# Kernel optimization log

Measured on AMD Instinct MI355X. Metric: run time of the kernel, lower is better.

## Reference

```python
import jax, jax.numpy as jnp
import numpy as np
import math

B, S, D_IN, D_ATTN, D_HID = 4, 2048, 1024, 1024, 1024

def gelu_erf(x):
    return 0.5 * x * (1.0 + jax.lax.erf(x / math.sqrt(2.0)))

def setup_inputs() -> dict:
    key = jax.random.key(0)
    k = jax.random.split(key, 8)
    inputs = jax.random.normal(k[0], (B, S, D_IN), dtype=jnp.float32)
    attn_mask = jax.random.randint(k[1], (B, S, S), 0, 2, dtype=jnp.int32)
    sq = 1.0 / math.sqrt(D_IN)
    Wq = jax.random.normal(k[2], (D_IN, D_ATTN), dtype=jnp.float32) * sq
    bq = jnp.zeros((D_ATTN,), dtype=jnp.float32)
    Wk = jax.random.normal(k[3], (D_IN, D_ATTN), dtype=jnp.float32) * sq
    bk = jnp.zeros((D_ATTN,), dtype=jnp.float32)
    Wv = jax.random.normal(k[4], (D_IN, D_HID), dtype=jnp.float32) * sq
    bv = jnp.zeros((D_HID,), dtype=jnp.float32)
    return {"inputs": inputs, "attn_mask": attn_mask,
            "Wq": Wq, "bq": bq, "Wk": Wk, "bk": bk, "Wv": Wv, "bv": bv}

def reference(inputs, attn_mask, Wq, bq, Wk, bk, Wv, bv):
    # Q, K: [B, S, d_k]
    Q = inputs @ Wq + bq
    K = inputs @ Wk + bk
    scores = jnp.einsum('bqd,bkd->bqk', Q, K) / math.sqrt(D_ATTN)
    scores = scores + attn_mask.astype(scores.dtype) * (-1e9)
    attn = jax.nn.softmax(scores, axis=-1)
    WV = gelu_erf(inputs @ Wv + bv)           # [B, S, hidden]
    context = jnp.einsum('bqk,bkh->bqh', attn, WV)
    return (context, attn)
```

## Files before the change

### kernel.cpp

```cpp
#include <hip/hip_runtime.h>
#include <hip/hip_bf16.h>
#include <math.h>

#define B_   4
#define S_   2048
#define DIN  1024
#define DATT 1024
#define DHID 1024

typedef short bf16x8 __attribute__((ext_vector_type(8)));
typedef float f32x4  __attribute__((ext_vector_type(4)));

__device__ inline unsigned short f2bf(float f) {
    unsigned u = __float_as_uint(f);
    u += 0x7fffu + ((u >> 16) & 1u);
    return (unsigned short)(u >> 16);
}
__device__ inline float bf2f(unsigned u16) {
    return __uint_as_float(u16 << 16);
}
__device__ inline void gld16(const void* g, void* l) {
    __builtin_amdgcn_global_load_lds(
        (const __attribute__((address_space(1))) unsigned int*)g,
        (__attribute__((address_space(3))) unsigned int*)l, 16, 0, 0);
}

__global__ __launch_bounds__(256)
void xcvt_k(const float* __restrict__ x, unsigned short* __restrict__ xb)
{
    int i = blockIdx.x * 256 + threadIdx.x;
    const float4* p = (const float4*)x + (size_t)i * 2;
    float4 v0 = p[0], v1 = p[1];
    uint4 o;
    o.x = (unsigned)f2bf(v0.x) | ((unsigned)f2bf(v0.y) << 16);
    o.y = (unsigned)f2bf(v0.z) | ((unsigned)f2bf(v0.w) << 16);
    o.z = (unsigned)f2bf(v1.x) | ((unsigned)f2bf(v1.y) << 16);
    o.w = (unsigned)f2bf(v1.z) | ((unsigned)f2bf(v1.w) << 16);
    ((uint4*)xb)[i] = o;
}

__global__ __launch_bounds__(256)
void wcvt_k(const float* __restrict__ Wq, const float* __restrict__ Wk,
            const float* __restrict__ Wv, unsigned short* __restrict__ Wt)
{
    int w = blockIdx.y;
    const float* W = (w == 0) ? Wq : ((w == 1) ? Wk : Wv);
    unsigned short* D = Wt + (size_t)w * DIN * DATT;
    int t = blockIdx.x * 256 + threadIdx.x;
    int n  = t >> 6;
    int kc = (t & 63) * 16;
    unsigned short r[16];
#pragma unroll
    for (int i = 0; i < 16; ++i) r[i] = f2bf(W[(size_t)(kc + i) * DATT + n]);
    uint4 o0, o1;
    o0.x = (unsigned)r[0] | ((unsigned)r[1] << 16);  o0.y = (unsigned)r[2] | ((unsigned)r[3] << 16);
    o0.z = (unsigned)r[4] | ((unsigned)r[5] << 16);  o0.w = (unsigned)r[6] | ((unsigned)r[7] << 16);
    o1.x = (unsigned)r[8] | ((unsigned)r[9] << 16);  o1.y = (unsigned)r[10] | ((unsigned)r[11] << 16);
    o1.z = (unsigned)r[12] | ((unsigned)r[13] << 16); o1.w = (unsigned)r[14] | ((unsigned)r[15] << 16);
    *(uint4*)(D + (size_t)n * DIN + kc)     = o0;
    *(uint4*)(D + (size_t)n * DIN + kc + 8) = o1;
}

template<int EPI>
__global__ __launch_bounds__(512, 2)
void gemm256_k(const unsigned short* __restrict__ Ap, const unsigned short* __restrict__ Bp,
               const float* __restrict__ b0, const float* __restrict__ b1,
               const float* __restrict__ b2, const int* __restrict__ maskp,
               void* __restrict__ Cp, void* __restrict__ Cp2,
               int K, int lda, int ldb, int ldc,
               long aStride, long bStride, long cStride, long mStride, float scale)
{
    __shared__ __align__(16) char ldsb[131072];

    const int tid  = threadIdx.x;
    const int z    = blockIdx.z;
    const int row0 = blockIdx.y * 256;
    const int col0 = blockIdx.x * 256;
    const int wid  = tid >> 6, lane = tid & 63;
    const int lr = lane & 15, lg = lane >> 4;
    const int wm = wid >> 2, wn = wid & 3;
    const int tw = (tid & 448) * 16;

    const unsigned short* Ab = Ap + (size_t)aStride * z;
    const unsigned short* Bb = Bp + (size_t)bStride * z;

    const int swzA = lr & 7;
    const int swzB = lg ^ ((lr >> 1) & 3);

    f32x4 acc[8][4] = {};
    const int nt = K >> 6;

#define STAGE_A(buf, k0n, r) {                                                  \
    int gr = (((r) & 1) << 7) + (((r) >> 1) << 6) + (tid >> 3);                 \
    int jj = (tid & 7) ^ (gr & 7);                                              \
    gld16(Ab + (size_t)(row0 + gr) * lda + (k0n) + jj * 8,                      \
          ldsb + (size_t)(buf) * 65536 + (r) * 8192 + tw); }

#define STAGE_B(buf, k0n, r) {                                                  \
    int rw = (((r) & 1) << 7) + (tid >> 2);                                     \
    int jj = (tid & 3) ^ ((rw >> 1) & 3);                                       \
    gld16(Bb + (size_t)(col0 + rw) * ldb + (k0n) + ((r) >> 1) * 32 + jj * 8,    \
          ldsb + (size_t)(buf) * 65536 + 32768 + ((r) >> 1) * 16384             \
               + (((r) & 1) << 13) + tw); }

#define PHASE(mh, kk, DOSTAGE) {                                                \
    const char* lb = ldsb + (size_t)cb * 65536;                                 \
    bf16x8 av[4], bv[4];                                                        \
    _Pragma("unroll")                                                           \
    for (int m = 0; m < 4; ++m) {                                               \
        int Rl = (mh) * 128 + wm * 64 + m * 16 + lr;                            \
        av[m] = *(const bf16x8*)(lb + Rl * 128 + ((((kk) * 4 + lg) ^ swzA) * 16)); \
    }                                                                           \
    _Pragma("unroll")                                                           \
    for (int n = 0; n < 4; ++n) {                                               \
        int Rb = wn * 64 + n * 16 + lr;                                         \
        bv[n] = *(const bf16x8*)(lb + 32768 + (kk) * 16384 + Rb * 64 + swzB * 16); \
    }                                                                           \
    DOSTAGE;                                                                    \
    asm volatile("s_waitcnt lgkmcnt(0)" ::: "memory");                          \
    __builtin_amdgcn_sched_barrier(0);                                          \
    __builtin_amdgcn_s_setprio(1);                                              \
    _Pragma("unroll")                                                           \
    for (int m = 0; m < 4; ++m)                                                 \
        _Pragma("unroll")                                                       \
        for (int n = 0; n < 4; ++n)                                             \
            acc[(mh) * 4 + m][n] = __builtin_amdgcn_mfma_f32_16x16x32_bf16(     \
                av[m], bv[n], acc[(mh) * 4 + m][n], 0, 0, 0);                   \
    __builtin_amdgcn_s_setprio(0); }

    STAGE_A(0, 0, 0); STAGE_B(0, 0, 0);
    STAGE_A(0, 0, 1); STAGE_B(0, 0, 1);
    STAGE_A(0, 0, 2); STAGE_A(0, 0, 3);
    STAGE_B(0, 0, 2); STAGE_B(0, 0, 3);

    int cb = 0;
    for (int t = 0; t < nt; ++t) {
        const bool pf = (t + 1) < nt;
        const int k0n = (t + 1) << 6;
        const int nb = cb ^ 1;
        asm volatile("s_waitcnt vmcnt(4)\ns_barrier" ::: "memory");
        PHASE(0, 0, if (pf) { STAGE_A(nb, k0n, 0); STAGE_B(nb, k0n, 0); })
        if (pf) asm volatile("s_waitcnt vmcnt(4)\ns_barrier" ::: "memory");
        else    asm volatile("s_waitcnt vmcnt(2)\ns_barrier" ::: "memory");
        PHASE(1, 0, if (pf) { STAGE_A(nb, k0n, 1); STAGE_B(nb, k0n, 1); })
        if (pf) asm volatile("s_waitcnt vmcnt(4)\ns_barrier" ::: "memory");
        else    asm volatile("s_waitcnt vmcnt(0)\ns_barrier" ::: "memory");
        PHASE(0, 1, if (pf) { STAGE_A(nb, k0n, 2); STAGE_A(nb, k0n, 3); })
        PHASE(1, 1, if (pf) { STAGE_B(nb, k0n, 2); STAGE_B(nb, k0n, 3); })
        cb = nb;
    }
#undef PHASE
#undef STAGE_A
#undef STAGE_B

    if (EPI == 6) {
        int w = col0 >> 10;
        int cb0 = (col0 & 1023) + wn * 64;
        if (w < 2) {
            unsigned short* C = (unsigned short*)Cp + (size_t)w * ((size_t)B_ * S_ * DATT);
            const float* bias = w ? b1 : b0;
#pragma unroll
            for (int ni = 0; ni < 4; ++ni) {
                int col = cb0 + ni * 16 + lr;
                float bb = bias[col];
#pragma unroll
                for (int mi = 0; mi < 8; ++mi) {
                    int rowb = row0 + wm * 128 + mi * 16 + lg * 4;
#pragma unroll
                    for (int v = 0; v < 4; ++v)
                        C[(size_t)(rowb + v) * DATT + col] = f2bf(acc[mi][ni][v] + bb);
                }
            }
        } else {
            unsigned short* C = (unsigned short*)Cp2;
            int zz = row0 >> 11;
            int sb = (row0 & 2047) + wm * 128;
#pragma unroll
            for (int ni = 0; ni < 4; ++ni) {
                int col = cb0 + ni * 16 + lr;
                float bb = b2[col];
#pragma unroll
                for (int mi = 0; mi < 8; ++mi) {
                    unsigned short r[4];
#pragma unroll
                    for (int v = 0; v < 4; ++v) {
                        float xv = acc[mi][ni][v] + bb;
                        xv = 0.5f * xv * (1.0f + erff(xv * 0.70710678118654752f));
                        r[v] = f2bf(xv);
                    }
                    uint2 o;
                    o.x = (unsigned)r[0] | ((unsigned)r[1] << 16);
                    o.y = (unsigned)r[2] | ((unsigned)r[3] << 16);
                    *(uint2*)(C + ((size_t)zz * DHID + col) * S_ + sb + mi * 16 + lg * 4) = o;
                }
            }
        }
    } else if (EPI == 4) {
        unsigned short* C = (unsigned short*)Cp + (size_t)cStride * z;
        const int* mp = maskp + (size_t)mStride * z;
#pragma unroll
        for (int mi = 0; mi < 8; ++mi) {
            int rowb = row0 + wm * 128 + mi * 16 + lg * 4;
#pragma unroll
            for (int ni = 0; ni < 4; ++ni) {
                int col = col0 + wn * 64 + ni * 16 + lr;
#pragma unroll
                for (int v = 0; v < 4; ++v) {
                    float sv = acc[mi][ni][v] * scale;
                    int mk = mp[(size_t)(rowb + v) * ldc + col];
                    float ev = mk ? 0.0f : __expf(sv);
                    C[(size_t)(rowb + v) * ldc + col] = f2bf(ev);
                }
            }
        }
    } else {
        float* C = (float*)Cp + (size_t)cStride * z;
        const float* invs = b0 + (size_t)z * S_;
#pragma unroll
        for (int mi = 0; mi < 8; ++mi) {
            int rowb = row0 + wm * 128 + mi * 16 + lg * 4;
#pragma unroll
            for (int ni = 0; ni < 4; ++ni) {
                int col = col0 + wn * 64 + ni * 16 + lr;
#pragma unroll
                for (int v = 0; v < 4; ++v)
                    C[(size_t)(rowb + v) * ldc + col] = acc[mi][ni][v] * invs[rowb + v];
            }
        }
    }
}

template<bool WRITEATTN>
__global__ __launch_bounds__(256)
void rownorm_k(const unsigned short* __restrict__ e, float* __restrict__ attn,
               float* __restrict__ invs)
{
    const int row = blockIdx.x;
    const int tid = threadIdx.x;
    uint4 u = ((const uint4*)(e + (size_t)row * S_))[tid];
    float f[8];
    f[0] = bf2f(u.x & 0xffffu); f[1] = bf2f(u.x >> 16);
    f[2] = bf2f(u.y & 0xffffu); f[3] = bf2f(u.y >> 16);
    f[4] = bf2f(u.z & 0xffffu); f[5] = bf2f(u.z >> 16);
    f[6] = bf2f(u.w & 0xffffu); f[7] = bf2f(u.w >> 16);
    float s = ((f[0] + f[1]) + (f[2] + f[3])) + ((f[4] + f[5]) + (f[6] + f[7]));
#pragma unroll
    for (int o = 32; o; o >>= 1) s += __shfl_xor(s, o);
    __shared__ float red[4];
    if ((tid & 63) == 0) red[tid >> 6] = s;
    __syncthreads();
    s = (red[0] + red[1]) + (red[2] + red[3]);
    float inv = 1.0f / s;
    if (WRITEATTN) {
        float* p = attn + (size_t)row * S_;
        ((float4*)p)[tid * 2]     = make_float4(f[0] * inv, f[1] * inv, f[2] * inv, f[3] * inv);
        ((float4*)p)[tid * 2 + 1] = make_float4(f[4] * inv, f[5] * inv, f[6] * inv, f[7] * inv);
    } else {
        if (tid == 0) invs[row] = inv;
    }
}

template<int AMODE, int EPI>
__global__ __launch_bounds__(256)
void gemm_k(const void* __restrict__ Ap, const unsigned short* __restrict__ Bp,
            const float* __restrict__ b0, const float* __restrict__ b1,
            const float* __restrict__ b2, const int* __restrict__ maskp,
            void* __restrict__ Cp, void* __restrict__ Cp2,
            int K, int lda, int ldb, int ldc,
            long aStride, long bStride, long cStride, long mStride, float scale)
{
    __shared__ __align__(16) unsigned short sh[2][2][128][64];
    const int tid  = threadIdx.x;
    const int z    = blockIdx.z;
    const int row0 = blockIdx.y * 128;
    const int col0 = blockIdx.x * 128;
    const int wave = tid >> 6, lane = tid & 63;
    const int lr = lane & 15, lg = lane >> 4;
    const int wm = (wave >> 1) * 64, wn = (wave & 1) * 64;
    const unsigned short* Bb = Bp + (size_t)bStride * z;
    f32x4 acc[4][4] = {};
    const int nt = K >> 6;
    auto stage = [&](int b, int k0) {
        if (AMODE == 0) {
            const unsigned short* A = (const unsigned short*)Ap + (size_t)aStride * z;
#pragma unroll
            for (int q = 0; q < 4; ++q) {
                int c = q * 256 + tid;
                int row = c >> 3, j = c & 7;
                gld16((const char*)(A + (size_t)(row0 + row) * lda + k0) + ((j ^ (row & 7)) << 4),
                      (char*)&sh[b][0][0][0] + ((q * 256 + (tid & 192)) << 4));
            }
        } else {
            const float* A = (const float*)Ap + (size_t)aStride * z;
#pragma unroll
            for (int q = 0; q < 4; ++q) {
                int c = q * 256 + tid;
                int row = c >> 3, j = c & 7;
                const float* src = A + (size_t)(row0 + row) * lda + k0 + ((j ^ (row & 7)) << 3);
                float4 v0 = *(const float4*)src;
                float4 v1 = *(const float4*)(src + 4);
                uint4 p;
                p.x = (unsigned)f2bf(v0.x) | ((unsigned)f2bf(v0.y) << 16);
                p.y = (unsigned)f2bf(v0.z) | ((unsigned)f2bf(v0.w) << 16);
                p.z = (unsigned)f2bf(v1.x) | ((unsigned)f2bf(v1.y) << 16);
                p.w = (unsigned)f2bf(v1.z) | ((unsigned)f2bf(v1.w) << 16);
                *(uint4*)((char*)&sh[b][0][0][0] + ((size_t)c << 4)) = p;
            }
        }
#pragma unroll
        for (int q = 0; q < 4; ++q) {
            int c = q * 256 + tid;
            int row = c >> 3, j = c & 7;
            gld16((const char*)(Bb + (size_t)(col0 + row) * ldb + k0) + ((j ^ (row & 7)) << 4),
                  (char*)&sh[b][1][0][0] + ((q * 256 + (tid & 192)) << 4));
        }
    };
    stage(0, 0);
    __syncthreads();
    int cur = 0;
    for (int t = 0; t < nt; ++t) {
        if (t + 1 < nt) stage(cur ^ 1, (t + 1) << 6);
        const char* baseA = (const char*)&sh[cur][0][0][0];
        const char* baseB = (const char*)&sh[cur][1][0][0];
        bf16x8 af[2][4], bfv[2][4];
#pragma unroll
        for (int s = 0; s < 2; ++s)
#pragma unroll
            for (int i = 0; i < 4; ++i) {
                int ra = wm + i * 16 + lr;
                af[s][i]  = *(const bf16x8*)(baseA + ra * 128 + ((((s << 2) | lg) ^ (ra & 7)) << 4));
                int rb = wn + i * 16 + lr;
                bfv[s][i] = *(const bf16x8*)(baseB + rb * 128 + ((((s << 2) | lg) ^ (rb & 7)) << 4));
            }
#pragma unroll
        for (int s = 0; s < 2; ++s)
#pragma unroll
            for (int mi = 0; mi < 4; ++mi)
#pragma unroll
                for (int ni = 0; ni < 4; ++ni)
                    acc[mi][ni] = __builtin_amdgcn_mfma_f32_16x16x32_bf16(af[s][mi], bfv[s][ni], acc[mi][ni], 0, 0, 0);
        if (t + 1 < nt) __syncthreads();
        cur ^= 1;
    }
    if (EPI == 6) {
        int w = col0 >> 10;
        int cb = (col0 & 1023) + wn;
        if (w < 2) {
            unsigned short* C = (unsigned short*)Cp + (size_t)w * ((size_t)B_ * S_ * DATT);
            const float* bias = w ? b1 : b0;
#pragma unroll
            for (int mi = 0; mi < 4; ++mi)
#pragma unroll
                for (int ni = 0; ni < 4; ++ni) {
                    int col = cb + ni * 16 + lr;
                    float bb = bias[col];
                    int rowb = row0 + wm + mi * 16 + lg * 4;
#pragma unroll
                    for (int v = 0; v < 4; ++v)
                        C[(size_t)(rowb + v) * DATT + col] = f2bf(acc[mi][ni][v] + bb);
                }
        } else {
            unsigned short* C = (unsigned short*)Cp2;
            int zz = row0 >> 11;
            int sb = (row0 & 2047) + wm;
#pragma unroll
            for (int mi = 0; mi < 4; ++mi)
#pragma unroll
                for (int ni = 0; ni < 4; ++ni) {
                    int col = cb + ni * 16 + lr;
                    float bb = b2[col];
                    unsigned short r[4];
#pragma unroll
                    for (int v = 0; v < 4; ++v) {
                        float xv = acc[mi][ni][v] + bb;
                        xv = 0.5f * xv * (1.0f + erff(xv * 0.70710678118654752f));
                        r[v] = f2bf(xv);
                    }
                    uint2 o;
                    o.x = (unsigned)r[0] | ((unsigned)r[1] << 16);
                    o.y = (unsigned)r[2] | ((unsigned)r[3] << 16);
                    *(uint2*)(C + ((size_t)zz * DHID + col) * S_ + sb + mi * 16 + lg * 4) = o;
                }
        }
    } else {
        float* C = (float*)Cp + (size_t)cStride * z;
        const int* mp = (EPI == 2) ? (maskp + (size_t)mStride * z) : nullptr;
#pragma unroll
        for (int mi = 0; mi < 4; ++mi)
#pragma unroll
            for (int ni = 0; ni < 4; ++ni) {
                int col = col0 + wn + ni * 16 + lr;
                int rowb = row0 + wm + mi * 16 + lg * 4;
#pragma unroll
                for (int v = 0; v < 4; ++v) {
                    float val = acc[mi][ni][v];
                    if (EPI == 2) val = val * scale + (float)mp[(size_t)(rowb + v) * ldc + col] * (-1e9f);
                    C[(size_t)(rowb + v) * ldc + col] = val;
                }
            }
    }
}

__global__ __launch_bounds__(256)
void softmax_k(float* __restrict__ attn)
{
    const int row = blockIdx.x;
    float* p = attn + (size_t)row * S_;
    const int tid = threadIdx.x;
    float4 a = ((const float4*)p)[tid * 2];
    float4 b = ((const float4*)p)[tid * 2 + 1];
    float m = fmaxf(fmaxf(fmaxf(a.x, a.y), fmaxf(a.z, a.w)),
                    fmaxf(fmaxf(b.x, b.y), fmaxf(b.z, b.w)));
#pragma unroll
    for (int o = 32; o; o >>= 1) m = fmaxf(m, __shfl_xor(m, o));
    __shared__ float redm[4];
    __shared__ float reds[4];
    if ((tid & 63) == 0) redm[tid >> 6] = m;
    __syncthreads();
    m = fmaxf(fmaxf(redm[0], redm[1]), fmaxf(redm[2], redm[3]));
    float e[8];
    e[0] = expf(a.x - m); e[1] = expf(a.y - m); e[2] = expf(a.z - m); e[3] = expf(a.w - m);
    e[4] = expf(b.x - m); e[5] = expf(b.y - m); e[6] = expf(b.z - m); e[7] = expf(b.w - m);
    float s = e[0] + e[1] + e[2] + e[3] + e[4] + e[5] + e[6] + e[7];
#pragma unroll
    for (int o = 32; o; o >>= 1) s += __shfl_xor(s, o);
    if ((tid & 63) == 0) reds[tid >> 6] = s;
    __syncthreads();
    s = reds[0] + reds[1] + reds[2] + reds[3];
    float inv = 1.0f / s;
    ((float4*)p)[tid * 2]     = make_float4(e[0] * inv, e[1] * inv, e[2] * inv, e[3] * inv);
    ((float4*)p)[tid * 2 + 1] = make_float4(e[4] * inv, e[5] * inv, e[6] * inv, e[7] * inv);
}

extern "C" void kernel_launch(void* const* d_in, const int* in_sizes, int n_in,
                              void* d_out, int out_size, void* d_ws, size_t ws_size,
                              hipStream_t stream)
{
    const float* x    = (const float*)d_in[0];
    const int*   mask = (const int*)d_in[1];
    const float* Wq   = (const float*)d_in[2];
    const float* bq   = (const float*)d_in[3];
    const float* Wk   = (const float*)d_in[4];
    const float* bk   = (const float*)d_in[5];
    const float* Wv   = (const float*)d_in[6];
    const float* bv   = (const float*)d_in[7];

    float* ctx  = (float*)d_out;
    float* attn = ctx + (size_t)B_ * S_ * DHID;

    unsigned short* Qb = (unsigned short*)ctx;
    unsigned short* Kb = Qb + (size_t)B_ * S_ * DATT;
    unsigned short* Xb   = (unsigned short*)attn;
    unsigned short* Wb   = Xb + (size_t)B_ * S_ * DIN;
    unsigned short* WVbT = Wb + (size_t)3 * DIN * DATT;

    const size_t eElems = (size_t)B_ * S_ * S_;
    bool fast = ws_size >= eElems * 2 + (size_t)B_ * S_ * 4 + 256;

    dim3 blk(256), blk5(512);

    xcvt_k<<<dim3(4096), blk, 0, stream>>>(x, Xb);
    wcvt_k<<<dim3(256, 3), blk, 0, stream>>>(Wq, Wk, Wv, Wb);

    if (fast) {
        unsigned short* e    = (unsigned short*)d_ws;
        float*          invs = (float*)(e + eElems);

        gemm256_k<6><<<dim3(12, 32, 1), blk5, 0, stream>>>(
            Xb, Wb, bq, bk, bv, nullptr, Qb, WVbT,
            DIN, DIN, DIN, 0, 0, 0, 0, 0, 1.0f);
        gemm256_k<4><<<dim3(8, 8, 4), blk5, 0, stream>>>(
            Qb, Kb, nullptr, nullptr, nullptr, mask, e, nullptr,
            DATT, DATT, DATT, S_,
            (long)S_ * DATT, (long)S_ * DATT, (long)S_ * S_, (long)S_ * S_, 0.03125f);
        rownorm_k<false><<<dim3(B_ * S_), blk, 0, stream>>>(e, nullptr, invs);
        gemm256_k<5><<<dim3(4, 8, 4), blk5, 0, stream>>>(
            e, WVbT, invs, nullptr, nullptr, nullptr, ctx, nullptr,
            S_, S_, S_, DHID,
            (long)S_ * S_, (long)DHID * S_, (long)S_ * DHID, 0, 1.0f);
        rownorm_k<true><<<dim3(B_ * S_), blk, 0, stream>>>(e, attn, nullptr);
    } else {
        unsigned short* WVw = (unsigned short*)d_ws;
        gemm_k<0, 6><<<dim3(24, 64, 1), blk, 0, stream>>>(
            Xb, Wb, bq, bk, bv, nullptr, Qb, WVw,
            DIN, DIN, DIN, 0, 0, 0, 0, 0, 1.0f);
        gemm_k<0, 2><<<dim3(16, 16, 4), blk, 0, stream>>>(
            Qb, Kb, nullptr, nullptr, nullptr, mask, attn, nullptr,
            DATT, DATT, DATT, S_,
            (long)S_ * DATT, (long)S_ * DATT, (long)S_ * S_, (long)S_ * S_, 0.03125f);
        softmax_k<<<dim3(B_ * S_), blk, 0, stream>>>(attn);
        gemm_k<1, 3><<<dim3(8, 16, 4), blk, 0, stream>>>(
            attn, WVw, nullptr, nullptr, nullptr, nullptr, ctx, nullptr,
            S_, S_, S_, DHID,
            (long)S_ * S_, (long)DHID * S_, (long)S_ * DHID, 0, 1.0f);
    }
}
```

Baseline: 243.0 us.

## Bit-pack attention mask, add 256x128 GEMM tile, reuse B fragments across phases

Adds a pre-pass that packs the int32 attention mask into one bit per element. The QK^T epilogue then reads 32x less mask data than the per-element int loads it replaces. The projection and context GEMMs move to a new 256x128 tile kernel with smaller LDS use, which doubles the grid size to fill more CUs. Both GEMM variants also reuse the B fragments loaded in the first M-half phase for the second, cutting redundant LDS reads. The costs are an extra kernel launch, more workspace, and lower per-block reuse in the narrower tile.

```diff
diff --git a/kernel.cpp b/kernel.cpp
--- a/kernel.cpp
+++ b/kernel.cpp
@@ -61,14 +61,28 @@
     *(uint4*)(D + (size_t)n * DIN + kc + 8) = o1;
 }
 
-template<int EPI>
+__global__ __launch_bounds__(256)
+void mpack_k(const int* __restrict__ m, unsigned* __restrict__ mb)
+{
+    int w = blockIdx.x * 256 + threadIdx.x;
+    const uint4* p = (const uint4*)(m + (size_t)w * 32);
+    unsigned bits = 0;
+#pragma unroll
+    for (int g = 0; g < 8; ++g) {
+        uint4 v = p[g];
+        bits |= (v.x ? 1u : 0u) << (g * 4 + 0);
+        bits |= (v.y ? 1u : 0u) << (g * 4 + 1);
+        bits |= (v.z ? 1u : 0u) << (g * 4 + 2);
+        bits |= (v.w ? 1u : 0u) << (g * 4 + 3);
+    }
+    mb[w] = bits;
+}
+
 __global__ __launch_bounds__(512, 2)
-void gemm256_k(const unsigned short* __restrict__ Ap, const unsigned short* __restrict__ Bp,
-               const float* __restrict__ b0, const float* __restrict__ b1,
-               const float* __restrict__ b2, const int* __restrict__ maskp,
-               void* __restrict__ Cp, void* __restrict__ Cp2,
-               int K, int lda, int ldb, int ldc,
-               long aStride, long bStride, long cStride, long mStride, float scale)
+void gemmA_k(const unsigned short* __restrict__ Ap, const unsigned short* __restrict__ Bp,
+             const unsigned* __restrict__ mbits, unsigned short* __restrict__ Cp,
+             int K, int lda, int ldb, int ldc,
+             long aStride, long bStride, long cStride, float scale)
 {
     __shared__ __align__(16) char ldsb[131072];
 
@@ -103,18 +117,20 @@
           ldsb + (size_t)(buf) * 65536 + 32768 + ((r) >> 1) * 16384             \
                + (((r) & 1) << 13) + tw); }
 
-#define PHASE(mh, kk, DOSTAGE) {                                                \
+#define PHASE_A(mh, kk, BV, LOADB, DOSTAGE) {                                   \
     const char* lb = ldsb + (size_t)cb * 65536;                                 \
-    bf16x8 av[4], bv[4];                                                        \
+    bf16x8 av[4];                                                               \
     _Pragma("unroll")                                                           \
     for (int m = 0; m < 4; ++m) {                                               \
         int Rl = (mh) * 128 + wm * 64 + m * 16 + lr;                            \
-        av[m] = *(const bf16x8*)(lb + Rl * 128 + ((((kk) * 4 + lg) ^ swzA) * 16)); \
+        av[m] = *(const bf16x8*)(lb + Rl * 128 + ((((kk) * 4 + lg) ^ swzA) << 4)); \
     }                                                                           \
-    _Pragma("unroll")                                                           \
-    for (int n = 0; n < 4; ++n) {                                               \
-        int Rb = wn * 64 + n * 16 + lr;                                         \
-        bv[n] = *(const bf16x8*)(lb + 32768 + (kk) * 16384 + Rb * 64 + swzB * 16); \
+    if (LOADB) {                                                                \
+        _Pragma("unroll")                                                       \
+        for (int n = 0; n < 4; ++n) {                                           \
+            int Rb = wn * 64 + n * 16 + lr;                                     \
+            BV[n] = *(const bf16x8*)(lb + 32768 + (kk) * 16384 + Rb * 64 + (swzB << 4)); \
+        }                                                                       \
     }                                                                           \
     DOSTAGE;                                                                    \
     asm volatile("s_waitcnt lgkmcnt(0)" ::: "memory");                          \
@@ -125,7 +141,7 @@
         _Pragma("unroll")                                                       \
         for (int n = 0; n < 4; ++n)                                             \
             acc[(mh) * 4 + m][n] = __builtin_amdgcn_mfma_f32_16x16x32_bf16(     \
-                av[m], bv[n], acc[(mh) * 4 + m][n], 0, 0, 0);                   \
+                av[m], BV[n], acc[(mh) * 4 + m][n], 0, 0, 0);                   \
     __builtin_amdgcn_s_setprio(0); }
 
     STAGE_A(0, 0, 0); STAGE_B(0, 0, 0);
@@ -138,20 +154,137 @@
         const bool pf = (t + 1) < nt;
         const int k0n = (t + 1) << 6;
         const int nb = cb ^ 1;
+        bf16x8 bv0[4], bv1[4];
         asm volatile("s_waitcnt vmcnt(4)\ns_barrier" ::: "memory");
-        PHASE(0, 0, if (pf) { STAGE_A(nb, k0n, 0); STAGE_B(nb, k0n, 0); })
+        PHASE_A(0, 0, bv0, true,  if (pf) { STAGE_A(nb, k0n, 0); STAGE_B(nb, k0n, 0); })
         if (pf) asm volatile("s_waitcnt vmcnt(4)\ns_barrier" ::: "memory");
         else    asm volatile("s_waitcnt vmcnt(2)\ns_barrier" ::: "memory");
-        PHASE(1, 0, if (pf) { STAGE_A(nb, k0n, 1); STAGE_B(nb, k0n, 1); })
+        PHASE_A(1, 0, bv0, false, if (pf) { STAGE_A(nb, k0n, 1); STAGE_B(nb, k0n, 1); })
         if (pf) asm volatile("s_waitcnt vmcnt(4)\ns_barrier" ::: "memory");
         else    asm volatile("s_waitcnt vmcnt(0)\ns_barrier" ::: "memory");
-        PHASE(0, 1, if (pf) { STAGE_A(nb, k0n, 2); STAGE_A(nb, k0n, 3); })
-        PHASE(1, 1, if (pf) { STAGE_B(nb, k0n, 2); STAGE_B(nb, k0n, 3); })
+        PHASE_A(0, 1, bv1, true,  if (pf) { STAGE_A(nb, k0n, 2); STAGE_A(nb, k0n, 3); })
+        PHASE_A(1, 1, bv1, false, if (pf) { STAGE_B(nb, k0n, 2); STAGE_B(nb, k0n, 3); })
         cb = nb;
     }
-#undef PHASE
+#undef PHASE_A
 #undef STAGE_A
 #undef STAGE_B
+
+    unsigned short* C = Cp + (size_t)cStride * z;
+    const unsigned* mb = mbits + (size_t)z * (S_ * S_ / 32);
+    const int wbase = (col0 + wn * 64) >> 5;
+#pragma unroll
+    for (int mi = 0; mi < 8; ++mi) {
+        int rowb = row0 + wm * 128 + mi * 16 + lg * 4;
+#pragma unroll
+        for (int v = 0; v < 4; ++v) {
+            int row = rowb + v;
+            unsigned w0 = mb[(size_t)row * (S_ / 32) + wbase];
+            unsigned w1 = mb[(size_t)row * (S_ / 32) + wbase + 1];
+#pragma unroll
+            for (int ni = 0; ni < 4; ++ni) {
+                int col = col0 + wn * 64 + ni * 16 + lr;
+                unsigned wsel = (ni & 2) ? w1 : w0;
+                float ev = ((wsel >> ((ni & 1) * 16 + lr)) & 1)
+                         ? 0.0f : __expf(acc[mi][ni][v] * scale);
+                C[(size_t)row * ldc + col] = f2bf(ev);
+            }
+        }
+    }
+}
+
+template<int EPI>
+__global__ __launch_bounds__(512, 2)
+void gemmB_k(const unsigned short* __restrict__ Ap, const unsigned short* __restrict__ Bp,
+             const float* __restrict__ b0, const float* __restrict__ b1,
+             const float* __restrict__ b2,
+             void* __restrict__ Cp, void* __restrict__ Cp2,
+             int K, int lda, int ldb, int ldc,
+             long aStride, long bStride, long cStride, float scale)
+{
+    __shared__ __align__(16) char ldsb[98304];
+
+    const int tid  = threadIdx.x;
+    const int z    = blockIdx.z;
+    const int row0 = blockIdx.y * 256;
+    const int col0 = blockIdx.x * 128;
+    const int wid  = tid >> 6, lane = tid & 63;
+    const int lr = lane & 15, lg = lane >> 4;
+    const int wm = wid >> 1, wn = wid & 1;
+    const int tw = (tid & 448) * 16;
+
+    const unsigned short* Ab = Ap + (size_t)aStride * z;
+    const unsigned short* Bb = Bp + (size_t)bStride * z;
+
+    const int swzA = lr & 7;
+    const int swzB = lg ^ ((lr >> 1) & 3);
+
+    f32x4 acc[4][4] = {};
+    const int nt = K >> 6;
+
+#define STAGE_AB(buf, k0n, m) {                                                 \
+    int fr = (tid >> 3) & 15, j = tid & 7;                                      \
+    int gr = ((tid >> 7) << 6) + (m) * 16 + fr;                                 \
+    gld16(Ab + (size_t)(row0 + gr) * lda + (k0n) + ((j ^ (fr & 7)) << 3),       \
+          ldsb + (size_t)(buf) * 49152 + (m) * 8192 + tw); }
+
+#define STAGE_BB(buf, k0n, kk) {                                                \
+    int rw = tid >> 2;                                                          \
+    int jj = (tid & 3) ^ ((rw >> 1) & 3);                                       \
+    gld16(Bb + (size_t)(col0 + rw) * ldb + (k0n) + (kk) * 32 + (jj << 3),       \
+          ldsb + (size_t)(buf) * 49152 + 32768 + (kk) * 8192 + tw); }
+
+#define PHASE_B(rh, kk, BV, LOADB, DOSTAGE) {                                   \
+    const char* lb = ldsb + (size_t)cb * 49152;                                 \
+    bf16x8 av[2];                                                               \
+    _Pragma("unroll")                                                           \
+    for (int mm = 0; mm < 2; ++mm) {                                            \
+        int m = (rh) * 2 + mm;                                                  \
+        av[mm] = *(const bf16x8*)(lb + m * 8192 + wm * 2048 + lr * 128          \
+                                  + ((((kk) * 4 + lg) ^ swzA) << 4));           \
+    }                                                                           \
+    if (LOADB) {                                                                \
+        _Pragma("unroll")                                                       \
+        for (int n = 0; n < 4; ++n) {                                           \
+            int Rb = wn * 64 + n * 16 + lr;                                     \
+            BV[n] = *(const bf16x8*)(lb + 32768 + (kk) * 8192 + Rb * 64 + (swzB << 4)); \
+        }                                                                       \
+    }                                                                           \
+    DOSTAGE;                                                                    \
+    asm volatile("s_waitcnt lgkmcnt(0)" ::: "memory");                          \
+    __builtin_amdgcn_sched_barrier(0);                                          \
+    __builtin_amdgcn_s_setprio(1);                                              \
+    _Pragma("unroll")                                                           \
+    for (int mm = 0; mm < 2; ++mm)                                              \
+        _Pragma("unroll")                                                       \
+        for (int n = 0; n < 4; ++n)                                             \
+            acc[(rh) * 2 + mm][n] = __builtin_amdgcn_mfma_f32_16x16x32_bf16(    \
+                av[mm], BV[n], acc[(rh) * 2 + mm][n], 0, 0, 0);                 \
+    __builtin_amdgcn_s_setprio(0); }
+
+    STAGE_AB(0, 0, 0); STAGE_AB(0, 0, 1); STAGE_BB(0, 0, 0);
+    STAGE_AB(0, 0, 2); STAGE_AB(0, 0, 3); STAGE_BB(0, 0, 1);
+
+    int cb = 0;
+    for (int t = 0; t < nt; ++t) {
+        const bool pf = (t + 1) < nt;
+        const int k0n = (t + 1) << 6;
+        const int nb = cb ^ 1;
+        bf16x8 bv0[4], bv1[4];
+        asm volatile("s_waitcnt vmcnt(3)\ns_barrier" ::: "memory");
+        PHASE_B(0, 0, bv0, true,  if (pf) { STAGE_AB(nb, k0n, 0); STAGE_AB(nb, k0n, 1); })
+        if (pf) asm volatile("s_waitcnt vmcnt(3)\ns_barrier" ::: "memory");
+        else    asm volatile("s_waitcnt vmcnt(1)\ns_barrier" ::: "memory");
+        PHASE_B(1, 0, bv0, false, if (pf) { STAGE_BB(nb, k0n, 0); })
+        if (pf) asm volatile("s_waitcnt vmcnt(3)\ns_barrier" ::: "memory");
+        else    asm volatile("s_waitcnt vmcnt(0)\ns_barrier" ::: "memory");
+        PHASE_B(0, 1, bv1, true,  if (pf) { STAGE_AB(nb, k0n, 2); STAGE_AB(nb, k0n, 3); })
+        PHASE_B(1, 1, bv1, false, if (pf) { STAGE_BB(nb, k0n, 1); })
+        cb = nb;
+    }
+#undef PHASE_B
+#undef STAGE_AB
+#undef STAGE_BB
 
     if (EPI == 6) {
         int w = col0 >> 10;
@@ -164,8 +297,8 @@
                 int col = cb0 + ni * 16 + lr;
                 float bb = bias[col];
 #pragma unroll
-                for (int mi = 0; mi < 8; ++mi) {
-                    int rowb = row0 + wm * 128 + mi * 16 + lg * 4;
+                for (int mi = 0; mi < 4; ++mi) {
+                    int rowb = row0 + wm * 64 + mi * 16 + lg * 4;
 #pragma unroll
                     for (int v = 0; v < 4; ++v)
                         C[(size_t)(rowb + v) * DATT + col] = f2bf(acc[mi][ni][v] + bb);
@@ -174,13 +307,13 @@
         } else {
             unsigned short* C = (unsigned short*)Cp2;
             int zz = row0 >> 11;
-            int sb = (row0 & 2047) + wm * 128;
+            int sb = (row0 & 2047) + wm * 64;
 #pragma unroll
             for (int ni = 0; ni < 4; ++ni) {
                 int col = cb0 + ni * 16 + lr;
                 float bb = b2[col];
 #pragma unroll
-                for (int mi = 0; mi < 8; ++mi) {
+                for (int mi = 0; mi < 4; ++mi) {
                     unsigned short r[4];
 #pragma unroll
                     for (int v = 0; v < 4; ++v) {
@@ -195,30 +328,12 @@
                 }
             }
         }
-    } else if (EPI == 4) {
-        unsigned short* C = (unsigned short*)Cp + (size_t)cStride * z;
-        const int* mp = maskp + (size_t)mStride * z;
-#pragma unroll
-        for (int mi = 0; mi < 8; ++mi) {
-            int rowb = row0 + wm * 128 + mi * 16 + lg * 4;
-#pragma unroll
-            for (int ni = 0; ni < 4; ++ni) {
-                int col = col0 + wn * 64 + ni * 16 + lr;
-#pragma unroll
-                for (int v = 0; v < 4; ++v) {
-                    float sv = acc[mi][ni][v] * scale;
-                    int mk = mp[(size_t)(rowb + v) * ldc + col];
-                    float ev = mk ? 0.0f : __expf(sv);
-                    C[(size_t)(rowb + v) * ldc + col] = f2bf(ev);
-                }
-            }
-        }
     } else {
         float* C = (float*)Cp + (size_t)cStride * z;
         const float* invs = b0 + (size_t)z * S_;
 #pragma unroll
-        for (int mi = 0; mi < 8; ++mi) {
-            int rowb = row0 + wm * 128 + mi * 16 + lg * 4;
+        for (int mi = 0; mi < 4; ++mi) {
+            int rowb = row0 + wm * 64 + mi * 16 + lg * 4;
 #pragma unroll
             for (int ni = 0; ni < 4; ++ni) {
                 int col = col0 + wn * 64 + ni * 16 + lr;
@@ -455,7 +570,8 @@
     unsigned short* WVbT = Wb + (size_t)3 * DIN * DATT;
 
     const size_t eElems = (size_t)B_ * S_ * S_;
-    bool fast = ws_size >= eElems * 2 + (size_t)B_ * S_ * 4 + 256;
+    const size_t mWords = (size_t)B_ * S_ * S_ / 32;
+    bool fast = ws_size >= eElems * 2 + (size_t)B_ * S_ * 4 + mWords * 4 + 256;
 
     dim3 blk(256), blk5(512);
 
@@ -465,19 +581,21 @@
     if (fast) {
         unsigned short* e    = (unsigned short*)d_ws;
         float*          invs = (float*)(e + eElems);
-
-        gemm256_k<6><<<dim3(12, 32, 1), blk5, 0, stream>>>(
-            Xb, Wb, bq, bk, bv, nullptr, Qb, WVbT,
-            DIN, DIN, DIN, 0, 0, 0, 0, 0, 1.0f);
-        gemm256_k<4><<<dim3(8, 8, 4), blk5, 0, stream>>>(
-            Qb, Kb, nullptr, nullptr, nullptr, mask, e, nullptr,
+        unsigned*       mb   = (unsigned*)(invs + (size_t)B_ * S_);
+
+        mpack_k<<<dim3(mWords / 256), blk, 0, stream>>>(mask, mb);
+        gemmB_k<6><<<dim3(24, 32, 1), blk5, 0, stream>>>(
+            Xb, Wb, bq, bk, bv, Qb, WVbT,
+            DIN, DIN, DIN, 0, 0, 0, 0, 1.0f);
+        gemmA_k<<<dim3(8, 8, 4), blk5, 0, stream>>>(
+            Qb, Kb, mb, e,
             DATT, DATT, DATT, S_,
-            (long)S_ * DATT, (long)S_ * DATT, (long)S_ * S_, (long)S_ * S_, 0.03125f);
+            (long)S_ * DATT, (long)S_ * DATT, (long)S_ * S_, 0.03125f);
         rownorm_k<false><<<dim3(B_ * S_), blk, 0, stream>>>(e, nullptr, invs);
-        gemm256_k<5><<<dim3(4, 8, 4), blk5, 0, stream>>>(
-            e, WVbT, invs, nullptr, nullptr, nullptr, ctx, nullptr,
+        gemmB_k<5><<<dim3(8, 8, 4), blk5, 0, stream>>>(
+            e, WVbT, invs, nullptr, nullptr, ctx, nullptr,
             S_, S_, S_, DHID,
-            (long)S_ * S_, (long)DHID * S_, (long)S_ * DHID, 0, 1.0f);
+            (long)S_ * S_, (long)DHID * S_, (long)S_ * DHID, 1.0f);
         rownorm_k<true><<<dim3(B_ * S_), blk, 0, stream>>>(e, attn, nullptr);
     } else {
         unsigned short* WVw = (unsigned short*)d_ws;
```

New measurement: 233.2 us. -4.1%, faster.

## Pack mask to bits, restructure 256-tile GEMM pipeline, use smaller GEMM for PV

Applied to the files above, without the earlier changes.

Adds a kernel that packs the int32 attention mask into one bit per element, so the QK^T epilogue reads 32x less mask data. The 256x256 GEMM is rewritten with a new LDS layout (32-wide K halves, triple-stage prefetch) and finer-grained phases that reuse B fragments across two M quarters, with barriers placed around each phase. The P·V GEMM moves from the 256 tile kernel to the older 128-tile gemm_k with a new EPI 5 epilogue. In exchange it adds an extra launch and workspace for the mask bits, more barriers per K step, and assumes nt is even.

```diff
diff --git a/kernel.cpp b/kernel.cpp
--- a/kernel.cpp
+++ b/kernel.cpp
@@ -61,14 +61,31 @@
     *(uint4*)(D + (size_t)n * DIN + kc + 8) = o1;
 }
 
+__global__ __launch_bounds__(256)
+void mpack_k(const int* __restrict__ m, unsigned* __restrict__ mb)
+{
+    int w = blockIdx.x * 256 + threadIdx.x;
+    const uint4* p = (const uint4*)(m + (size_t)w * 32);
+    unsigned bits = 0;
+#pragma unroll
+    for (int g = 0; g < 8; ++g) {
+        uint4 v = p[g];
+        bits |= (v.x ? 1u : 0u) << (g * 4 + 0);
+        bits |= (v.y ? 1u : 0u) << (g * 4 + 1);
+        bits |= (v.z ? 1u : 0u) << (g * 4 + 2);
+        bits |= (v.w ? 1u : 0u) << (g * 4 + 3);
+    }
+    mb[w] = bits;
+}
+
 template<int EPI>
 __global__ __launch_bounds__(512, 2)
-void gemm256_k(const unsigned short* __restrict__ Ap, const unsigned short* __restrict__ Bp,
-               const float* __restrict__ b0, const float* __restrict__ b1,
-               const float* __restrict__ b2, const int* __restrict__ maskp,
-               void* __restrict__ Cp, void* __restrict__ Cp2,
-               int K, int lda, int ldb, int ldc,
-               long aStride, long bStride, long cStride, long mStride, float scale)
+void gemmP_k(const unsigned short* __restrict__ Ap, const unsigned short* __restrict__ Bp,
+             const float* __restrict__ b0, const float* __restrict__ b1,
+             const float* __restrict__ b2, const unsigned* __restrict__ mbits,
+             void* __restrict__ Cp, void* __restrict__ Cp2,
+             int K, int lda, int ldb, int ldc,
+             long aStride, long bStride, long cStride, float scale)
 {
     __shared__ __align__(16) char ldsb[131072];
 
@@ -79,79 +96,83 @@
     const int wid  = tid >> 6, lane = tid & 63;
     const int lr = lane & 15, lg = lane >> 4;
     const int wm = wid >> 2, wn = wid & 3;
-    const int tw = (tid & 448) * 16;
+    const int twv  = (tid & 448) * 16;
+    const int sl16 = (lg ^ ((lr >> 1) & 3)) << 4;
+    const int sj   = (tid & 3) ^ ((tid >> 3) & 3);
 
     const unsigned short* Ab = Ap + (size_t)aStride * z;
     const unsigned short* Bb = Bp + (size_t)bStride * z;
 
-    const int swzA = lr & 7;
-    const int swzB = lg ^ ((lr >> 1) & 3);
-
     f32x4 acc[8][4] = {};
     const int nt = K >> 6;
 
-#define STAGE_A(buf, k0n, r) {                                                  \
-    int gr = (((r) & 1) << 7) + (((r) >> 1) << 6) + (tid >> 3);                 \
-    int jj = (tid & 7) ^ (gr & 7);                                              \
-    gld16(Ab + (size_t)(row0 + gr) * lda + (k0n) + jj * 8,                      \
-          ldsb + (size_t)(buf) * 65536 + (r) * 8192 + tw); }
-
-#define STAGE_B(buf, k0n, r) {                                                  \
-    int rw = (((r) & 1) << 7) + (tid >> 2);                                     \
-    int jj = (tid & 3) ^ ((rw >> 1) & 3);                                       \
-    gld16(Bb + (size_t)(col0 + rw) * ldb + (k0n) + ((r) >> 1) * 32 + jj * 8,    \
-          ldsb + (size_t)(buf) * 65536 + 32768 + ((r) >> 1) * 16384             \
-               + (((r) & 1) << 13) + tw); }
-
-#define PHASE(mh, kk, DOSTAGE) {                                                \
-    const char* lb = ldsb + (size_t)cb * 65536;                                 \
-    bf16x8 av[4], bv[4];                                                        \
-    _Pragma("unroll")                                                           \
-    for (int m = 0; m < 4; ++m) {                                               \
-        int Rl = (mh) * 128 + wm * 64 + m * 16 + lr;                            \
-        av[m] = *(const bf16x8*)(lb + Rl * 128 + ((((kk) * 4 + lg) ^ swzA) * 16)); \
+#define STA(kk, buf, kt) {                                                      \
+    int gr0 = tid >> 2;                                                         \
+    gld16(Ab + (size_t)(row0 + gr0) * lda + (kt) * 64 + (kk) * 32 + sj * 8,     \
+          ldsb + (buf) * 32768 + (kk) * 16384 + twv);                           \
+    gld16(Ab + (size_t)(row0 + 128 + gr0) * lda + (kt) * 64 + (kk) * 32 + sj * 8, \
+          ldsb + (buf) * 32768 + (kk) * 16384 + 8192 + twv); }
+
+#define STB(kk, buf, kt) {                                                      \
+    int gr0 = tid >> 2;                                                         \
+    gld16(Bb + (size_t)(col0 + gr0) * ldb + (kt) * 64 + (kk) * 32 + sj * 8,     \
+          ldsb + 65536 + (buf) * 32768 + (kk) * 16384 + twv);                   \
+    gld16(Bb + (size_t)(col0 + 128 + gr0) * ldb + (kt) * 64 + (kk) * 32 + sj * 8, \
+          ldsb + 65536 + (buf) * 32768 + (kk) * 16384 + 8192 + twv); }
+
+#define PH(buf, kk, mq, BV, LOADB, STG, DOVM) {                                 \
+    const char* as_ = ldsb + (buf) * 32768 + (kk) * 16384;                      \
+    const char* bs_ = ldsb + 65536 + (buf) * 32768 + (kk) * 16384;              \
+    bf16x8 a0_, a1_, a2_, a3_;                                                  \
+    a0_ = *(const bf16x8*)(as_ + (wm * 128 + (mq) * 64 +  0 + lr) * 64 + sl16); \
+    a1_ = *(const bf16x8*)(as_ + (wm * 128 + (mq) * 64 + 16 + lr) * 64 + sl16); \
+    a2_ = *(const bf16x8*)(as_ + (wm * 128 + (mq) * 64 + 32 + lr) * 64 + sl16); \
+    a3_ = *(const bf16x8*)(as_ + (wm * 128 + (mq) * 64 + 48 + lr) * 64 + sl16); \
+    if (LOADB) {                                                                \
+        BV[0] = *(const bf16x8*)(bs_ + (wn * 64 +  0 + lr) * 64 + sl16);        \
+        BV[1] = *(const bf16x8*)(bs_ + (wn * 64 + 16 + lr) * 64 + sl16);        \
+        BV[2] = *(const bf16x8*)(bs_ + (wn * 64 + 32 + lr) * 64 + sl16);        \
+        BV[3] = *(const bf16x8*)(bs_ + (wn * 64 + 48 + lr) * 64 + sl16);        \
     }                                                                           \
-    _Pragma("unroll")                                                           \
-    for (int n = 0; n < 4; ++n) {                                               \
-        int Rb = wn * 64 + n * 16 + lr;                                         \
-        bv[n] = *(const bf16x8*)(lb + 32768 + (kk) * 16384 + Rb * 64 + swzB * 16); \
-    }                                                                           \
-    DOSTAGE;                                                                    \
+    STG;                                                                        \
+    __builtin_amdgcn_s_barrier();                                               \
     asm volatile("s_waitcnt lgkmcnt(0)" ::: "memory");                          \
     __builtin_amdgcn_sched_barrier(0);                                          \
     __builtin_amdgcn_s_setprio(1);                                              \
     _Pragma("unroll")                                                           \
-    for (int m = 0; m < 4; ++m)                                                 \
-        _Pragma("unroll")                                                       \
-        for (int n = 0; n < 4; ++n)                                             \
-            acc[(mh) * 4 + m][n] = __builtin_amdgcn_mfma_f32_16x16x32_bf16(     \
-                av[m], bv[n], acc[(mh) * 4 + m][n], 0, 0, 0);                   \
-    __builtin_amdgcn_s_setprio(0); }
-
-    STAGE_A(0, 0, 0); STAGE_B(0, 0, 0);
-    STAGE_A(0, 0, 1); STAGE_B(0, 0, 1);
-    STAGE_A(0, 0, 2); STAGE_A(0, 0, 3);
-    STAGE_B(0, 0, 2); STAGE_B(0, 0, 3);
-
-    int cb = 0;
-    for (int t = 0; t < nt; ++t) {
-        const bool pf = (t + 1) < nt;
-        const int k0n = (t + 1) << 6;
-        const int nb = cb ^ 1;
-        asm volatile("s_waitcnt vmcnt(4)\ns_barrier" ::: "memory");
-        PHASE(0, 0, if (pf) { STAGE_A(nb, k0n, 0); STAGE_B(nb, k0n, 0); })
-        if (pf) asm volatile("s_waitcnt vmcnt(4)\ns_barrier" ::: "memory");
-        else    asm volatile("s_waitcnt vmcnt(2)\ns_barrier" ::: "memory");
-        PHASE(1, 0, if (pf) { STAGE_A(nb, k0n, 1); STAGE_B(nb, k0n, 1); })
-        if (pf) asm volatile("s_waitcnt vmcnt(4)\ns_barrier" ::: "memory");
-        else    asm volatile("s_waitcnt vmcnt(0)\ns_barrier" ::: "memory");
-        PHASE(0, 1, if (pf) { STAGE_A(nb, k0n, 2); STAGE_A(nb, k0n, 3); })
-        PHASE(1, 1, if (pf) { STAGE_B(nb, k0n, 2); STAGE_B(nb, k0n, 3); })
-        cb = nb;
-    }
-#undef PHASE
-#undef STAGE_A
-#undef STAGE_B
+    for (int n = 0; n < 4; ++n) {                                               \
+        acc[(mq)*4+0][n] = __builtin_amdgcn_mfma_f32_16x16x32_bf16(a0_, BV[n], acc[(mq)*4+0][n], 0,0,0); \
+        acc[(mq)*4+1][n] = __builtin_amdgcn_mfma_f32_16x16x32_bf16(a1_, BV[n], acc[(mq)*4+1][n], 0,0,0); \
+        acc[(mq)*4+2][n] = __builtin_amdgcn_mfma_f32_16x16x32_bf16(a2_, BV[n], acc[(mq)*4+2][n], 0,0,0); \
+        acc[(mq)*4+3][n] = __builtin_amdgcn_mfma_f32_16x16x32_bf16(a3_, BV[n], acc[(mq)*4+3][n], 0,0,0); \
+    }                                                                           \
+    __builtin_amdgcn_s_setprio(0);                                              \
+    DOVM;                                                                       \
+    __builtin_amdgcn_s_barrier(); }
+
+    STA(0, 0, 0); STB(0, 0, 0);
+    STA(1, 0, 0); STB(1, 0, 0);
+    STA(0, 1, 1); STB(0, 1, 1);
+    asm volatile("s_waitcnt vmcnt(4)" ::: "memory");
+    __builtin_amdgcn_s_barrier();
+
+    for (int i = 0; i < (nt >> 1); ++i) {
+        int t1 = 2 * i + 1;
+        int t2 = 2 * i + 2; if (t2 > nt - 1) t2 = nt - 1;
+        int t3 = 2 * i + 3; if (t3 > nt - 1) t3 = nt - 1;
+        bf16x8 bv0[4], bv1[4];
+        PH(0, 0, 0, bv0, true,  { STA(1, 1, t1); }, {})
+        PH(0, 0, 1, bv0, false, { STB(1, 1, t1); }, { asm volatile("s_waitcnt vmcnt(8)" ::: "memory"); })
+        PH(0, 1, 0, bv1, true,  { STA(0, 0, t2); }, {})
+        PH(0, 1, 1, bv1, false, { STB(0, 0, t2); }, { asm volatile("s_waitcnt vmcnt(8)" ::: "memory"); })
+        PH(1, 0, 0, bv0, true,  { STA(1, 0, t2); }, {})
+        PH(1, 0, 1, bv0, false, { STB(1, 0, t2); }, { asm volatile("s_waitcnt vmcnt(8)" ::: "memory"); })
+        PH(1, 1, 0, bv1, true,  { STA(0, 1, t3); }, {})
+        PH(1, 1, 1, bv1, false, { STB(0, 1, t3); }, { asm volatile("s_waitcnt vmcnt(8)" ::: "memory"); })
+    }
+#undef PH
+#undef STA
+#undef STB
 
     if (EPI == 6) {
         int w = col0 >> 10;
@@ -195,68 +216,28 @@
                 }
             }
         }
-    } else if (EPI == 4) {
+    } else {
         unsigned short* C = (unsigned short*)Cp + (size_t)cStride * z;
-        const int* mp = maskp + (size_t)mStride * z;
+        const unsigned* mb = mbits + (size_t)z * (S_ * S_ / 32);
+        const int wbase = (col0 + wn * 64) >> 5;
 #pragma unroll
         for (int mi = 0; mi < 8; ++mi) {
             int rowb = row0 + wm * 128 + mi * 16 + lg * 4;
 #pragma unroll
-            for (int ni = 0; ni < 4; ++ni) {
-                int col = col0 + wn * 64 + ni * 16 + lr;
-#pragma unroll
-                for (int v = 0; v < 4; ++v) {
-                    float sv = acc[mi][ni][v] * scale;
-                    int mk = mp[(size_t)(rowb + v) * ldc + col];
-                    float ev = mk ? 0.0f : __expf(sv);
-                    C[(size_t)(rowb + v) * ldc + col] = f2bf(ev);
+            for (int v = 0; v < 4; ++v) {
+                int row = rowb + v;
+                unsigned w0 = mb[(size_t)row * (S_ / 32) + wbase];
+                unsigned w1 = mb[(size_t)row * (S_ / 32) + wbase + 1];
+#pragma unroll
+                for (int ni = 0; ni < 4; ++ni) {
+                    int col = col0 + wn * 64 + ni * 16 + lr;
+                    unsigned wsel = (ni & 2) ? w1 : w0;
+                    float ev = ((wsel >> ((ni & 1) * 16 + lr)) & 1)
+                             ? 0.0f : __expf(acc[mi][ni][v] * scale);
+                    C[(size_t)row * ldc + col] = f2bf(ev);
                 }
             }
         }
-    } else {
-        float* C = (float*)Cp + (size_t)cStride * z;
-        const float* invs = b0 + (size_t)z * S_;
-#pragma unroll
-        for (int mi = 0; mi < 8; ++mi) {
-            int rowb = row0 + wm * 128 + mi * 16 + lg * 4;
-#pragma unroll
-            for (int ni = 0; ni < 4; ++ni) {
-                int col = col0 + wn * 64 + ni * 16 + lr;
-#pragma unroll
-                for (int v = 0; v < 4; ++v)
-                    C[(size_t)(rowb + v) * ldc + col] = acc[mi][ni][v] * invs[rowb + v];
-            }
-        }
-    }
-}
-
-template<bool WRITEATTN>
-__global__ __launch_bounds__(256)
-void rownorm_k(const unsigned short* __restrict__ e, float* __restrict__ attn,
-               float* __restrict__ invs)
-{
-    const int row = blockIdx.x;
-    const int tid = threadIdx.x;
-    uint4 u = ((const uint4*)(e + (size_t)row * S_))[tid];
-    float f[8];
-    f[0] = bf2f(u.x & 0xffffu); f[1] = bf2f(u.x >> 16);
-    f[2] = bf2f(u.y & 0xffffu); f[3] = bf2f(u.y >> 16);
-    f[4] = bf2f(u.z & 0xffffu); f[5] = bf2f(u.z >> 16);
-    f[6] = bf2f(u.w & 0xffffu); f[7] = bf2f(u.w >> 16);
-    float s = ((f[0] + f[1]) + (f[2] + f[3])) + ((f[4] + f[5]) + (f[6] + f[7]));
-#pragma unroll
-    for (int o = 32; o; o >>= 1) s += __shfl_xor(s, o);
-    __shared__ float red[4];
-    if ((tid & 63) == 0) red[tid >> 6] = s;
-    __syncthreads();
-    s = (red[0] + red[1]) + (red[2] + red[3]);
-    float inv = 1.0f / s;
-    if (WRITEATTN) {
-        float* p = attn + (size_t)row * S_;
-        ((float4*)p)[tid * 2]     = make_float4(f[0] * inv, f[1] * inv, f[2] * inv, f[3] * inv);
-        ((float4*)p)[tid * 2 + 1] = make_float4(f[4] * inv, f[5] * inv, f[6] * inv, f[7] * inv);
-    } else {
-        if (tid == 0) invs[row] = inv;
     }
 }
 
@@ -382,6 +363,19 @@
                     *(uint2*)(C + ((size_t)zz * DHID + col) * S_ + sb + mi * 16 + lg * 4) = o;
                 }
         }
+    } else if (EPI == 5) {
+        float* C = (float*)Cp + (size_t)cStride * z;
+        const float* invs = b0 + (size_t)z * S_;
+#pragma unroll
+        for (int mi = 0; mi < 4; ++mi)
+#pragma unroll
+            for (int ni = 0; ni < 4; ++ni) {
+                int col = col0 + wn + ni * 16 + lr;
+                int rowb = row0 + wm + mi * 16 + lg * 4;
+#pragma unroll
+                for (int v = 0; v < 4; ++v)
+                    C[(size_t)(rowb + v) * ldc + col] = acc[mi][ni][v] * invs[rowb + v];
+            }
     } else {
         float* C = (float*)Cp + (size_t)cStride * z;
         const int* mp = (EPI == 2) ? (maskp + (size_t)mStride * z) : nullptr;
@@ -398,6 +392,36 @@
                     C[(size_t)(rowb + v) * ldc + col] = val;
                 }
             }
+    }
+}
+
+template<bool WRITEATTN>
+__global__ __launch_bounds__(256)
+void rownorm_k(const unsigned short* __restrict__ e, float* __restrict__ attn,
+               float* __restrict__ invs)
+{
+    const int row = blockIdx.x;
+    const int tid = threadIdx.x;
+    uint4 u = ((const uint4*)(e + (size_t)row * S_))[tid];
+    float f[8];
+    f[0] = bf2f(u.x & 0xffffu); f[1] = bf2f(u.x >> 16);
+    f[2] = bf2f(u.y & 0xffffu); f[3] = bf2f(u.y >> 16);
+    f[4] = bf2f(u.z & 0xffffu); f[5] = bf2f(u.z >> 16);
+    f[6] = bf2f(u.w & 0xffffu); f[7] = bf2f(u.w >> 16);
+    float s = ((f[0] + f[1]) + (f[2] + f[3])) + ((f[4] + f[5]) + (f[6] + f[7]));
+#pragma unroll
+    for (int o = 32; o; o >>= 1) s += __shfl_xor(s, o);
+    __shared__ float red[4];
+    if ((tid & 63) == 0) red[tid >> 6] = s;
+    __syncthreads();
+    s = (red[0] + red[1]) + (red[2] + red[3]);
+    float inv = 1.0f / s;
+    if (WRITEATTN) {
+        float* p = attn + (size_t)row * S_;
+        ((float4*)p)[tid * 2]     = make_float4(f[0] * inv, f[1] * inv, f[2] * inv, f[3] * inv);
+        ((float4*)p)[tid * 2 + 1] = make_float4(f[4] * inv, f[5] * inv, f[6] * inv, f[7] * inv);
+    } else {
+        if (tid == 0) invs[row] = inv;
     }
 }
 
@@ -455,7 +479,8 @@
     unsigned short* WVbT = Wb + (size_t)3 * DIN * DATT;
 
     const size_t eElems = (size_t)B_ * S_ * S_;
-    bool fast = ws_size >= eElems * 2 + (size_t)B_ * S_ * 4 + 256;
+    const size_t mWords = (size_t)B_ * S_ * S_ / 32;
+    bool fast = ws_size >= eElems * 2 + (size_t)B_ * S_ * 4 + mWords * 4 + 256;
 
     dim3 blk(256), blk5(512);
 
@@ -465,16 +490,18 @@
     if (fast) {
         unsigned short* e    = (unsigned short*)d_ws;
         float*          invs = (float*)(e + eElems);
-
-        gemm256_k<6><<<dim3(12, 32, 1), blk5, 0, stream>>>(
+        unsigned*       mb   = (unsigned*)(invs + (size_t)B_ * S_);
+
+        mpack_k<<<dim3(mWords / 256), blk, 0, stream>>>(mask, mb);
+        gemmP_k<6><<<dim3(12, 32, 1), blk5, 0, stream>>>(
             Xb, Wb, bq, bk, bv, nullptr, Qb, WVbT,
-            DIN, DIN, DIN, 0, 0, 0, 0, 0, 1.0f);
-        gemm256_k<4><<<dim3(8, 8, 4), blk5, 0, stream>>>(
-            Qb, Kb, nullptr, nullptr, nullptr, mask, e, nullptr,
+            DIN, DIN, DIN, 0, 0, 0, 0, 1.0f);
+        gemmP_k<4><<<dim3(8, 8, 4), blk5, 0, stream>>>(
+            Qb, Kb, nullptr, nullptr, nullptr, mb, e, nullptr,
             DATT, DATT, DATT, S_,
-            (long)S_ * DATT, (long)S_ * DATT, (long)S_ * S_, (long)S_ * S_, 0.03125f);
+            (long)S_ * DATT, (long)S_ * DATT, (long)S_ * S_, 0.03125f);
         rownorm_k<false><<<dim3(B_ * S_), blk, 0, stream>>>(e, nullptr, invs);
-        gemm256_k<5><<<dim3(4, 8, 4), blk5, 0, stream>>>(
+        gemm_k<0, 5><<<dim3(8, 16, 4), blk, 0, stream>>>(
             e, WVbT, invs, nullptr, nullptr, nullptr, ctx, nullptr,
             S_, S_, S_, DHID,
             (long)S_ * S_, (long)DHID * S_, (long)S_ * DHID, 0, 1.0f);
```

New measurement: 240.4 us. About the same (-1.1%).
